# Optimization experiments

Measured on AMD Instinct MI355X. Metric: run time of the kernel, lower is better.

The kernel has to match this reference:

```python
import jax, jax.numpy as jnp
import numpy as np

HEAD_DIM = 128
NUM_HEADS = 16
NUM_KV_HEADS = 16
ROPE_MAX_POS = 4096
ROPE_BASE = 10000.0


def _rope_tables(seq_len):
    # cos/sin cached tables: [S, D/2]
    inv_freq = 1.0 / (ROPE_BASE ** (jnp.arange(0, HEAD_DIM, 2, dtype=jnp.float32) / HEAD_DIM))
    t = jnp.arange(seq_len, dtype=jnp.float32)
    freqs = jnp.outer(t, inv_freq)
    return jnp.cos(freqs), jnp.sin(freqs)


def _apply_rope(x, cos, sin):
    # x: [B, S, H, D]; cos/sin: [S, D/2] -> broadcast over heads as [S, 1, D/2]
    orig_dtype = x.dtype
    c = cos[:, None, :]
    s = sin[:, None, :]
    xf = x.astype(jnp.float32)
    x_real, x_im = jnp.split(xf, 2, axis=-1)  # half-split (not interleaved) RoPE
    x_real_e = x_real * c - x_im * s
    x_im_e = x_im * c + x_real * s
    return jnp.concatenate((x_real_e, x_im_e), axis=-1).astype(orig_dtype)


def setup_inputs() -> dict:
    key = jax.random.key(0)
    k1, k2, k3 = jax.random.split(key, 3)
    B, S, H = 1, 4096, 2048
    hidden_states = jax.random.normal(k1, (B, S, H), dtype=jnp.float32)
    # trunc-normal-ish init, std ~ 1/sqrt(fan_in)
    w_qkv = jax.random.normal(k2, ((NUM_HEADS + 2 * NUM_KV_HEADS) * HEAD_DIM, H), dtype=jnp.float32) / jnp.sqrt(jnp.float32(H))
    w_o = jax.random.normal(k3, (H, NUM_HEADS * HEAD_DIM), dtype=jnp.float32) / jnp.sqrt(jnp.float32(NUM_HEADS * HEAD_DIM))
    return {"hidden_states": hidden_states, "w_qkv": w_qkv, "w_o": w_o}


def reference(hidden_states, w_qkv, w_o):
    B, S, _ = hidden_states.shape
    qkv = jnp.einsum('bsh,oh->bso', hidden_states, w_qkv)
    qkv = qkv.reshape(B, S, NUM_HEADS + 2 * NUM_KV_HEADS, HEAD_DIM)
    q = qkv[:, :, :NUM_HEADS]
    k = qkv[:, :, NUM_HEADS:NUM_HEADS + NUM_KV_HEADS]
    v = qkv[:, :, NUM_HEADS + NUM_KV_HEADS:]

    cos, sin = _rope_tables(S)
    q = _apply_rope(q, cos, sin)
    k = _apply_rope(k, cos, sin)

    scale = 1.0 / jnp.sqrt(jnp.float32(HEAD_DIM)).astype(q.dtype)
    # scores: [B, H, Sq, Sk]
    scores = jnp.einsum('bqhd,bkhd->bhqk', q, k) * scale
    causal = jnp.tril(jnp.ones((S, S), dtype=bool))
    scores = jnp.where(causal[None, None], scores, jnp.finfo(scores.dtype).min)
    probs = jax.nn.softmax(scores, axis=-1)
    attn = jnp.einsum('bhqk,bkhd->bqhd', probs, v)
    attn = attn.reshape(B, S, NUM_HEADS * HEAD_DIM)
    return jnp.einsum('bso,ho->bsh', attn, w_o)
```

## Files before the change

### kernel.cpp

```cpp
#include <hip/hip_runtime.h>

typedef __bf16 bf16;
typedef __bf16 bf16x8 __attribute__((ext_vector_type(8)));
typedef __bf16 bf16x4 __attribute__((ext_vector_type(4)));
typedef float f32x4 __attribute__((ext_vector_type(4)));

#define SEQ 4096
#define QKV_LD 6144
#define HNUM 16

__device__ __forceinline__ void async16(const bf16* g, bf16* l) {
    __builtin_amdgcn_global_load_lds((const __attribute__((address_space(1))) void*)g,
                                     (__attribute__((address_space(3))) void*)l, 16, 0, 0);
}

__global__ __launch_bounds__(256) void prep(const float* __restrict__ X, bf16* __restrict__ Xb,
                                            const float* __restrict__ Wq, bf16* __restrict__ Wqb,
                                            const float* __restrict__ Wo, bf16* __restrict__ Wob,
                                            float* __restrict__ T) {
    const int b = blockIdx.x, t = threadIdx.x;
    if (b < 12288) {
        const float* src;
        bf16* dst;
        int off;
        if (b < 4096)       { src = X;  dst = Xb;  off = b; }
        else if (b < 10240) { src = Wq; dst = Wqb; off = b - 4096; }
        else                { src = Wo; dst = Wob; off = b - 10240; }
        int i = (off * 256 + t) * 8;
        f32x4 a = *(const f32x4*)(src + i);
        f32x4 c = *(const f32x4*)(src + i + 4);
        bf16x8 w;
#pragma unroll
        for (int j = 0; j < 4; j++) { w[j] = (bf16)a[j]; w[4 + j] = (bf16)c[j]; }
        *(bf16x8*)(dst + i) = w;
    } else {
        int i = (b - 12288) * 256 + t;
        int s = i >> 6, d = i & 63;
        float inv_freq = powf(10000.0f, -(float)d * (1.0f / 64.0f));
        float ang = (float)s * inv_freq;
        T[2 * i]     = cosf(ang);
        T[2 * i + 1] = sinf(ang);
    }
}

__device__ __forceinline__ bf16x8 ldfrag(const bf16* slot, int row, int qd) {
    int lin  = row * 64 + qd * 16;
    int phys = lin ^ (((lin >> 9) & 1) << 5);
    return *(const bf16x8*)((const char*)slot + phys);
}

#define STAGE2(SG, SGR0, STT, SKK, SBUF, SMAT)                                  \
    {                                                                           \
        int tcl = (STT) < NT ? (STT) : NT - 1;                                  \
        const bf16* gsrc = (SG) + (size_t)(SGR0)*K + tcl * 64 + (SKK)*32;       \
        bf16* sl = &LDS[SBUF][SMAT][SKK][0];                                    \
        async16(gsrc + g0, (bf16*)((char*)sl + lb0));                           \
        async16(gsrc + g1, (bf16*)((char*)sl + lb1));                           \
    }

#define PHASE(QM, KKI, LOADB, SG, SGR0, STT, SKK, SBUF, SMAT, DOVM)             \
    {                                                                           \
        if (LOADB) {                                                            \
            _Pragma("unroll") for (int j = 0; j < 4; j++)                       \
                bB[j] = ldfrag(&LDS[bi][1][KKI][0],                             \
                               (wc >> 1) * 128 + (wc & 1) * 32 +                \
                                   (j & 1) * 16 + (j >> 1) * 64 + ln, qd);      \
        }                                                                       \
        bf16x8 aA[4];                                                           \
        _Pragma("unroll") for (int i = 0; i < 4; i++)                           \
            aA[i] = ldfrag(&LDS[bi][0][KKI][0],                                 \
                           wr * 128 + (QM)*64 + i * 16 + ln, qd);               \
        STAGE2(SG, SGR0, STT, SKK, SBUF, SMAT);                                 \
        __builtin_amdgcn_sched_barrier(0);                                      \
        if (DOVM) {                                                             \
            asm volatile("s_waitcnt vmcnt(4)" ::: "memory");                    \
            __builtin_amdgcn_sched_barrier(0);                                  \
        }                                                                       \
        __builtin_amdgcn_s_barrier();                                           \
        __builtin_amdgcn_sched_barrier(0);                                      \
        __builtin_amdgcn_s_setprio(1);                                          \
        _Pragma("unroll") for (int i = 0; i < 4; i++)                           \
            _Pragma("unroll") for (int j = 0; j < 4; j++)                       \
                acc[(QM)*4 + i][j] = __builtin_amdgcn_mfma_f32_16x16x32_bf16(   \
                    aA[i], bB[j], acc[(QM)*4 + i][j], 0, 0, 0);                 \
        __builtin_amdgcn_s_setprio(0);                                          \
        __builtin_amdgcn_sched_barrier(0);                                      \
        __builtin_amdgcn_s_barrier();                                           \
        __builtin_amdgcn_sched_barrier(0);                                      \
    }

template <int ROPE>
__global__ __launch_bounds__(512, 2) void gemm256_nt(const bf16* __restrict__ A,
                                                     const bf16* __restrict__ B,
                                                     bf16* __restrict__ C,
                                                     int M, int N, int K,
                                                     const float* __restrict__ T) {
    __shared__ __align__(16) bf16 LDS[2][2][2][256 * 32];
    const int tid  = threadIdx.x;
    const int wave = tid >> 6, lane = tid & 63;
    const int qd = lane >> 4, ln = lane & 15;
    const int wr = wave >> 2, wc = wave & 3;
    const int bm = blockIdx.x * 256, bn = blockIdx.y * 256;
    const int NT = K >> 6;

    const int seg0 = wave * 2, seg1 = seg0 + 1;
    const int Pr0 = seg0 * 1024 + lane * 16;
    const int Pr1 = seg1 * 1024 + lane * 16;
    const int Lr0 = Pr0 ^ (((Pr0 >> 9) & 1) << 5);
    const int Lr1 = Pr1 ^ (((Pr1 >> 9) & 1) << 5);
    const size_t g0 = (size_t)(Lr0 >> 6) * K + ((Lr0 & 63) >> 1);
    const size_t g1 = (size_t)(Lr1 >> 6) * K + ((Lr1 & 63) >> 1);
    const int lb0 = seg0 * 1024, lb1 = seg1 * 1024;

    f32x4 acc[8][4] = {};

    STAGE2(A, bm, 0, 0, 0, 0);
    STAGE2(B, bn, 0, 0, 0, 1);
    STAGE2(A, bm, 0, 1, 0, 0);
    STAGE2(B, bn, 0, 1, 0, 1);
    STAGE2(A, bm, 1, 0, 1, 0);
    STAGE2(B, bn, 1, 0, 1, 1);
    __builtin_amdgcn_sched_barrier(0);
    asm volatile("s_waitcnt vmcnt(4)" ::: "memory");
    __builtin_amdgcn_sched_barrier(0);
    __builtin_amdgcn_s_barrier();
    __builtin_amdgcn_sched_barrier(0);

    for (int t = 0; t < NT; ++t) {
        const int bi = t & 1;
        bf16x8 bB[4];
        PHASE(0, 0, 1, A, bm, t + 1, 1, bi ^ 1, 0, 0)
        PHASE(1, 0, 0, B, bn, t + 1, 1, bi ^ 1, 1, 0)
        PHASE(0, 1, 1, A, bm, t + 2, 0, bi,     0, 0)
        PHASE(1, 1, 0, B, bn, t + 2, 0, bi,     1, 1)
    }
    asm volatile("s_waitcnt vmcnt(0)" ::: "memory");

    const int colb = bn + (wc >> 1) * 128 + (wc & 1) * 32 + ln;
    if (ROPE && bn < 4096) {
        const float2* T2 = (const float2*)T;
        const int d0 = (wc & 1) * 32 + ln;
#pragma unroll
        for (int mi = 0; mi < 8; mi++)
#pragma unroll
            for (int r = 0; r < 4; r++) {
                int row = bm + wr * 128 + mi * 16 + qd * 4 + r;
                float2 cs0 = T2[(size_t)row * 64 + d0];
                float2 cs1 = T2[(size_t)row * 64 + d0 + 16];
                float a0 = acc[mi][0][r], b0 = acc[mi][2][r];
                float a1 = acc[mi][1][r], b1 = acc[mi][3][r];
                size_t o = (size_t)row * N + colb;
                C[o]      = (bf16)(a0 * cs0.x - b0 * cs0.y);
                C[o + 64] = (bf16)(b0 * cs0.x + a0 * cs0.y);
                C[o + 16] = (bf16)(a1 * cs1.x - b1 * cs1.y);
                C[o + 80] = (bf16)(b1 * cs1.x + a1 * cs1.y);
            }
    } else if (ROPE) {
        bf16* Vb = C + 4096;
#pragma unroll
        for (int mi = 0; mi < 8; mi++) {
            const int row = bm + wr * 128 + mi * 16 + qd * 4;
            const int rhi = row >> 11;
            const int rlo = row & 2047;
#pragma unroll
            for (int j = 0; j < 4; j++) {
                const int dh = colb - 4096 + (j & 1) * 16 + (j >> 1) * 64;
                bf16x4 w;
#pragma unroll
                for (int r = 0; r < 4; r++) w[r] = (bf16)acc[mi][j][r];
                *(bf16x4*)(Vb + (size_t)(2 * dh + rhi) * N + rlo) = w;
            }
        }
    } else {
#pragma unroll
        for (int mi = 0; mi < 8; mi++)
#pragma unroll
            for (int r = 0; r < 4; r++) {
                size_t o = (size_t)(bm + wr * 128 + mi * 16 + qd * 4 + r) * N + colb;
                C[o]      = (bf16)acc[mi][0][r];
                C[o + 16] = (bf16)acc[mi][1][r];
                C[o + 64] = (bf16)acc[mi][2][r];
                C[o + 80] = (bf16)acc[mi][3][r];
            }
    }
}

__device__ __forceinline__ bf16x8 ldfragB(const bf16* slot, int row, int qd) {
    int lin  = row * 64 + qd * 16;
    int phys = lin ^ (((lin >> 9) & 1) << 5);
    return *(const bf16x8*)((const char*)slot + phys);
}

#define STG(TT, KKI, BUF)                                                      \
    {                                                                          \
        int tcl = (TT) < NT ? (TT) : NT - 1;                                   \
        const bf16* As = A + (size_t)bm * K + tcl * 64 + (KKI)*32;             \
        const bf16* Bs = B + (size_t)bn * K + tcl * 64 + (KKI)*32;             \
        async16(As + gA,  (bf16*)((char*)&LA[BUF][KKI][0] + lbA));             \
        async16(Bs + gB0, (bf16*)((char*)&LB[BUF][KKI][0] + lbB0));            \
        async16(Bs + gB1, (bf16*)((char*)&LB[BUF][KKI][0] + lbB1));            \
    }

#define PH(KKI, TT, SKK, SBUF, DOVM)                                           \
    {                                                                          \
        bf16x8 aA[4], bB[4];                                                   \
        _Pragma("unroll") for (int i = 0; i < 4; i++)                          \
            aA[i] = ldfragB(&LA[bi][KKI][0], wr * 64 + i * 16 + ln, qd);       \
        _Pragma("unroll") for (int j = 0; j < 4; j++)                          \
            bB[j] = ldfragB(&LB[bi][KKI][0], wc * 64 + j * 16 + ln, qd);       \
        STG(TT, SKK, SBUF);                                                    \
        __builtin_amdgcn_sched_barrier(0);                                     \
        if (DOVM) {                                                            \
            asm volatile("s_waitcnt vmcnt(3)" ::: "memory");                   \
            __builtin_amdgcn_sched_barrier(0);                                 \
        }                                                                      \
        __builtin_amdgcn_s_barrier();                                          \
        __builtin_amdgcn_sched_barrier(0);                                     \
        __builtin_amdgcn_s_setprio(1);                                         \
        _Pragma("unroll") for (int i = 0; i < 4; i++)                          \
            _Pragma("unroll") for (int j = 0; j < 4; j++)                      \
                acc[i][j] = __builtin_amdgcn_mfma_f32_16x16x32_bf16(           \
                    aA[i], bB[j], acc[i][j], 0, 0, 0);                         \
        __builtin_amdgcn_s_setprio(0);                                         \
        __builtin_amdgcn_sched_barrier(0);                                     \
        __builtin_amdgcn_s_barrier();                                          \
        __builtin_amdgcn_sched_barrier(0);                                     \
    }

template <int C_F32>
__global__ __launch_bounds__(512, 2) void gemm128x256(const bf16* __restrict__ A,
                                                      const bf16* __restrict__ B,
                                                      void* __restrict__ Cp,
                                                      int M, int N, int K) {
    __shared__ __align__(16) bf16 LA[2][2][128 * 32];
    __shared__ __align__(16) bf16 LB[2][2][256 * 32];
    const int tid  = threadIdx.x;
    const int wave = tid >> 6, lane = tid & 63;
    const int qd = lane >> 4, ln = lane & 15;
    const int wr = wave >> 2, wc = wave & 3;
    const int bm = blockIdx.x * 128, bn = blockIdx.y * 256;
    const int NT = K >> 6;

    const int PrA  = wave * 1024 + lane * 16;
    const int PrB0 = (2 * wave) * 1024 + lane * 16;
    const int PrB1 = PrB0 + 1024;
    const int LrA  = PrA  ^ (((PrA  >> 9) & 1) << 5);
    const int LrB0 = PrB0 ^ (((PrB0 >> 9) & 1) << 5);
    const int LrB1 = PrB1 ^ (((PrB1 >> 9) & 1) << 5);
    const size_t gA  = (size_t)(LrA  >> 6) * K + ((LrA  & 63) >> 1);
    const size_t gB0 = (size_t)(LrB0 >> 6) * K + ((LrB0 & 63) >> 1);
    const size_t gB1 = (size_t)(LrB1 >> 6) * K + ((LrB1 & 63) >> 1);
    const int lbA = wave * 1024, lbB0 = 2 * wave * 1024, lbB1 = lbB0 + 1024;

    f32x4 acc[4][4] = {};

    STG(0, 0, 0);
    STG(0, 1, 0);
    STG(1, 0, 1);
    __builtin_amdgcn_sched_barrier(0);
    asm volatile("s_waitcnt vmcnt(3)" ::: "memory");
    __builtin_amdgcn_sched_barrier(0);
    __builtin_amdgcn_s_barrier();
    __builtin_amdgcn_sched_barrier(0);

    for (int t = 0; t < NT; ++t) {
        const int bi = t & 1;
        PH(0, t + 1, 1, bi ^ 1, 0)
        PH(1, t + 2, 0, bi,     1)
    }
    asm volatile("s_waitcnt vmcnt(0)" ::: "memory");

    const size_t cb = (size_t)(bm + wr * 64 + qd * 4) * N + (bn + wc * 64 + ln);
#pragma unroll
    for (int mi = 0; mi < 4; mi++)
#pragma unroll
        for (int j = 0; j < 4; j++)
#pragma unroll
            for (int r = 0; r < 4; r++) {
                size_t idx = cb + (size_t)(mi * 16 + r) * N + j * 16;
                if (C_F32) ((float*)Cp)[idx] = acc[mi][j][r];
                else       ((bf16*)Cp)[idx]  = (bf16)acc[mi][j][r];
            }
}

template <int A_F32, int B_F32, int C_F32>
__global__ __launch_bounds__(256) void gemm_nt(const void* __restrict__ Ap,
                                               const void* __restrict__ Bp,
                                               void* __restrict__ Cp,
                                               int M, int N, int K) {
    __shared__ __align__(16) bf16 sA[128 * 32];
    __shared__ __align__(16) bf16 sB[128 * 32];
    const int tid  = threadIdx.x;
    const int wave = tid >> 6, lane = tid & 63;
    const int qd = lane >> 4, ln = lane & 15;
    const int bm = blockIdx.x * 128, bn = blockIdx.y * 128;
    const int wm = (wave >> 1) * 64, wn = (wave & 1) * 64;

    const int srow = wave * 16 + (lane >> 2);
    const int scol = (lane & 3) * 8;
    const size_t rowoff = (size_t)srow * K + scol;
    const size_t rowskip = (size_t)64 * K;

    const bf16* Ab = (const bf16*)Ap + (size_t)bm * K + rowoff;
    const bf16* Bb = (const bf16*)Bp + (size_t)bn * K + rowoff;
    const float* Af = (const float*)Ap + (size_t)bm * K + rowoff;
    const float* Bf = (const float*)Bp + (size_t)bn * K + rowoff;
    bf16* sAd0 = &sA[(wave * 16) * 32];
    bf16* sAd1 = &sA[(64 + wave * 16) * 32];
    bf16* sBd0 = &sB[(wave * 16) * 32];
    bf16* sBd1 = &sB[(64 + wave * 16) * 32];
    bf16* sAw0 = &sA[srow * 32 + scol];
    bf16* sAw1 = &sA[(64 + srow) * 32 + scol];
    bf16* sBw0 = &sB[srow * 32 + scol];
    bf16* sBw1 = &sB[(64 + srow) * 32 + scol];

    f32x4 acc[4][4] = {};
    for (int k0 = 0; k0 < K; k0 += 32) {
        if (A_F32) {
            f32x4 u0 = *(const f32x4*)(Af + k0);
            f32x4 u1 = *(const f32x4*)(Af + k0 + 4);
            f32x4 u2 = *(const f32x4*)(Af + rowskip + k0);
            f32x4 u3 = *(const f32x4*)(Af + rowskip + k0 + 4);
            bf16x8 w0, w1;
#pragma unroll
            for (int i = 0; i < 4; i++) { w0[i] = (bf16)u0[i]; w0[4 + i] = (bf16)u1[i];
                                          w1[i] = (bf16)u2[i]; w1[4 + i] = (bf16)u3[i]; }
            *(bf16x8*)sAw0 = w0;
            *(bf16x8*)sAw1 = w1;
        } else {
            async16(Ab + k0, sAd0);
            async16(Ab + rowskip + k0, sAd1);
        }
        if (B_F32) {
            f32x4 u0 = *(const f32x4*)(Bf + k0);
            f32x4 u1 = *(const f32x4*)(Bf + k0 + 4);
            f32x4 u2 = *(const f32x4*)(Bf + rowskip + k0);
            f32x4 u3 = *(const f32x4*)(Bf + rowskip + k0 + 4);
            bf16x8 w0, w1;
#pragma unroll
            for (int i = 0; i < 4; i++) { w0[i] = (bf16)u0[i]; w0[4 + i] = (bf16)u1[i];
                                          w1[i] = (bf16)u2[i]; w1[4 + i] = (bf16)u3[i]; }
            *(bf16x8*)sBw0 = w0;
            *(bf16x8*)sBw1 = w1;
        } else {
            async16(Bb + k0, sBd0);
            async16(Bb + rowskip + k0, sBd1);
        }
        __syncthreads();
        bf16x8 af[4], bfr[4];
#pragma unroll
        for (int i = 0; i < 4; i++)
            af[i] = *(const bf16x8*)&sA[(wm + i * 16 + ln) * 32 + qd * 8];
#pragma unroll
        for (int j = 0; j < 4; j++)
            bfr[j] = *(const bf16x8*)&sB[(wn + j * 16 + ln) * 32 + qd * 8];
#pragma unroll
        for (int i = 0; i < 4; i++)
#pragma unroll
            for (int j = 0; j < 4; j++)
                acc[i][j] = __builtin_amdgcn_mfma_f32_16x16x32_bf16(af[i], bfr[j], acc[i][j], 0, 0, 0);
        __syncthreads();
    }
    const size_t cbase = (size_t)(bm + wm + qd * 4) * N + (bn + wn + ln);
#pragma unroll
    for (int i = 0; i < 4; i++)
#pragma unroll
        for (int j = 0; j < 4; j++)
#pragma unroll
            for (int r = 0; r < 4; r++) {
                size_t idx = cbase + (size_t)(i * 16 + r) * N + j * 16;
                if (C_F32) ((float*)Cp)[idx] = acc[i][j][r];
                else       ((bf16*)Cp)[idx] = (bf16)acc[i][j][r];
            }
}

__global__ __launch_bounds__(256) void rope_k_inline(bf16* __restrict__ QKV) {
    const int s  = blockIdx.x;
    const int t  = threadIdx.x;
    const int hh = (blockIdx.y << 2) + (t >> 6);
    const int d  = t & 63;
    bf16* p = QKV + (size_t)s * QKV_LD + hh * 128 + d;
    float x0 = (float)p[0];
    float x1 = (float)p[64];
    float inv_freq = powf(10000.0f, -(float)d * (1.0f / 64.0f));
    float ang = (float)s * inv_freq;
    float c = cosf(ang), sn = sinf(ang);
    p[0]  = (bf16)(x0 * c - x1 * sn);
    p[64] = (bf16)(x1 * c + x0 * sn);
}

template <int USE_VT>
__global__ __launch_bounds__(256, 2) void flash_attn(const bf16* __restrict__ QKV,
                                                     bf16* __restrict__ O) {
    __shared__ __align__(16) bf16 sK[64 * 128];
    __shared__ __align__(16) bf16 sV[128 * 64];
    __shared__ __align__(16) bf16 sP[4][32 * 64];
    const int tid  = threadIdx.x;
    const int wave = tid >> 6, lane = tid & 63;
    const int qd = lane >> 4, ln = lane & 15;
    const int h  = blockIdx.x;
    const int y  = blockIdx.y;
    const int qtile = (y < 16) ? (31 - y) : (y - 16);
    const int qw0 = qtile * 128 + wave * 32;
    const int nkv = 2 * qtile + 2;
    const float scale = 0.08838834764831843f;

    bf16x8 Qf[2][4];
#pragma unroll
    for (int qt = 0; qt < 2; qt++) {
        const bf16* Qg = QKV + (size_t)(qw0 + qt * 16 + ln) * QKV_LD + h * 128;
#pragma unroll
        for (int ks = 0; ks < 4; ks++) {
            bf16x8 q8 = *(const bf16x8*)(Qg + ks * 32 + qd * 8);
#pragma unroll
            for (int e = 0; e < 8; e++) q8[e] = (bf16)((float)q8[e] * scale);
            Qf[qt][ks] = q8;
        }
    }

    f32x4 Oacc[2][8] = {};
    float l_i[2] = {0.0f, 0.0f};

    const int krow = tid >> 4;
    const int kblk = tid & 15;
    const int vrow = tid >> 3;
    const int vblk = tid & 7;
    const int vd   = tid & 127;
    const int vh   = tid >> 7;
    const bf16* Kg  = QKV + 2048 + h * 128;
    const bf16* Vg  = QKV + 4096 + h * 128;
    const bf16* Vtb = QKV + 4096;

    bf16x8 Kpre[4], Vpre[4];
#pragma unroll
    for (int rr = 0; rr < 4; rr++)
        Kpre[rr] = *(const bf16x8*)(Kg + (size_t)(rr * 16 + krow) * QKV_LD + kblk * 8);
    if (USE_VT) {
#pragma unroll
        for (int u = 0; u < 4; u++) {
            int dh = h * 128 + u * 32 + vrow;
            Vpre[u] = *(const bf16x8*)(Vtb + (size_t)(2 * dh) * QKV_LD + vblk * 8);
        }
    } else {
#pragma unroll
        for (int u = 0; u < 4; u++)
#pragma unroll
            for (int j = 0; j < 8; j++)
                Vpre[u][j] = Vg[(size_t)(vh * 32 + u * 8 + j) * QKV_LD + vd];
    }

    for (int kt = 0; kt < nkv; kt++) {
        const int kbase = kt * 64;
#pragma unroll
        for (int rr = 0; rr < 4; rr++) {
            int kv = rr * 16 + krow;
            *(bf16x8*)&sK[kv * 128 + ((kblk ^ (kv & 7)) * 8)] = Kpre[rr];
        }
        if (USE_VT) {
#pragma unroll
            for (int u = 0; u < 4; u++) {
                int d = u * 32 + vrow;
                *(bf16x8*)&sV[d * 64 + ((vblk ^ (d & 7)) * 8)] = Vpre[u];
            }
        } else {
#pragma unroll
            for (int u = 0; u < 4; u++)
                *(bf16x8*)&sV[vd * 64 + (((vh * 4 + u) ^ (vd & 7)) * 8)] = Vpre[u];
        }
        __syncthreads();
        if (kt + 1 < nkv) {
            const int nb = kbase + 64;
#pragma unroll
            for (int rr = 0; rr < 4; rr++)
                Kpre[rr] = *(const bf16x8*)(Kg + (size_t)(nb + rr * 16 + krow) * QKV_LD + kblk * 8);
            if (USE_VT) {
#pragma unroll
                for (int u = 0; u < 4; u++) {
                    int dh = h * 128 + u * 32 + vrow;
                    Vpre[u] = *(const bf16x8*)(Vtb + (size_t)(2 * dh + (nb >> 11)) * QKV_LD +
                                               (nb & 2047) + vblk * 8);
                }
            } else {
#pragma unroll
                for (int u = 0; u < 4; u++)
#pragma unroll
                    for (int j = 0; j < 8; j++)
                        Vpre[u][j] = Vg[(size_t)(nb + vh * 32 + u * 8 + j) * QKV_LD + vd];
            }
        }
        if (kbase <= qw0 + 31) {
            f32x4 Sacc[2][4] = {};
            __builtin_amdgcn_s_setprio(1);
#pragma unroll
            for (int ks = 0; ks < 4; ks++)
#pragma unroll
                for (int j = 0; j < 4; j++) {
                    bf16x8 af = *(const bf16x8*)&sK[(j * 16 + ln) * 128 + (((ks * 4 + qd) ^ (ln & 7)) * 8)];
                    Sacc[0][j] = __builtin_amdgcn_mfma_f32_16x16x32_bf16(af, Qf[0][ks], Sacc[0][j], 0, 0, 0);
                    Sacc[1][j] = __builtin_amdgcn_mfma_f32_16x16x32_bf16(af, Qf[1][ks], Sacc[1][j], 0, 0, 0);
                }
            __builtin_amdgcn_s_setprio(0);
#pragma unroll
            for (int qt = 0; qt < 2; qt++) {
                const int qs = qw0 + qt * 16;
                if (kbase + 63 > qs) {
#pragma unroll
                    for (int j = 0; j < 4; j++)
#pragma unroll
                        for (int r = 0; r < 4; r++)
                            if (kbase + j * 16 + qd * 4 + r > qs + ln) Sacc[qt][j][r] = -1e30f;
                }
                float psum = 0.0f;
#pragma unroll
                for (int j = 0; j < 4; j++) {
                    bf16x4 p4;
#pragma unroll
                    for (int r = 0; r < 4; r++) {
                        float p = __expf(Sacc[qt][j][r]);
                        psum += p;
                        p4[r] = (bf16)p;
                    }
                    int blk = (j * 2 + (qd >> 1)) ^ (ln & 7);
                    *(bf16x4*)&sP[wave][(qt * 16 + ln) * 64 + blk * 8 + (qd & 1) * 4] = p4;
                }
                psum += __shfl_xor(psum, 16);
                psum += __shfl_xor(psum, 32);
                l_i[qt] += psum;
            }
            __builtin_amdgcn_s_setprio(1);
#pragma unroll
            for (int ks = 0; ks < 2; ks++) {
                bf16x8 pf0 = *(const bf16x8*)&sP[wave][(0 * 16 + ln) * 64 + (((ks * 4 + qd) ^ (ln & 7)) * 8)];
                bf16x8 pf1 = *(const bf16x8*)&sP[wave][(1 * 16 + ln) * 64 + (((ks * 4 + qd) ^ (ln & 7)) * 8)];
#pragma unroll
                for (int dt = 0; dt < 8; dt++) {
                    bf16x8 vf = *(const bf16x8*)&sV[(dt * 16 + ln) * 64 + (((ks * 4 + qd) ^ (ln & 7)) * 8)];
                    Oacc[0][dt] = __builtin_amdgcn_mfma_f32_16x16x32_bf16(pf0, vf, Oacc[0][dt], 0, 0, 0);
                    Oacc[1][dt] = __builtin_amdgcn_mfma_f32_16x16x32_bf16(pf1, vf, Oacc[1][dt], 0, 0, 0);
                }
            }
            __builtin_amdgcn_s_setprio(0);
        }
        __syncthreads();
    }
#pragma unroll
    for (int qt = 0; qt < 2; qt++) {
        float linv[4];
#pragma unroll
        for (int r = 0; r < 4; r++)
            linv[r] = 1.0f / __shfl(l_i[qt], (lane & 48) | (qd * 4 + r));
        bf16* Ob = O + (size_t)(qw0 + qt * 16 + qd * 4) * 2048 + h * 128 + ln;
#pragma unroll
        for (int dt = 0; dt < 8; dt++)
#pragma unroll
            for (int r = 0; r < 4; r++)
                Ob[(size_t)r * 2048 + dt * 16] = (bf16)(Oacc[qt][dt][r] * linv[r]);
    }
}

extern "C" void kernel_launch(void* const* d_in, const int* in_sizes, int n_in,
                              void* d_out, int out_size, void* d_ws, size_t ws_size,
                              hipStream_t stream) {
    const float* X    = (const float*)d_in[0];
    const float* Wqkv = (const float*)d_in[1];
    const float* Wo   = (const float*)d_in[2];
    float* out = (float*)d_out;
    bf16* QKV = (bf16*)d_ws;
    bf16* ATT = QKV + (size_t)4096 * 6144;

    const size_t nX = (size_t)4096 * 2048, nWq = (size_t)6144 * 2048, nWo = (size_t)2048 * 2048;
    const size_t need = (nX * 3 + nWq * 2 + nWo) * 2 + nX * 2;

    if (ws_size >= need) {
        bf16* Xb  = ATT + nX;
        bf16* Wqb = Xb + nX;
        bf16* Wob = Wqb + nWq;
        float* Tab = (float*)ATT;
        prep<<<13312, 256, 0, stream>>>(X, Xb, Wqkv, Wqb, Wo, Wob, Tab);
        gemm256_nt<1><<<dim3(16, 24), 512, 0, stream>>>(Xb, Wqb, QKV, 4096, 6144, 2048, Tab);
        flash_attn<1><<<dim3(HNUM, 32), 256, 0, stream>>>(QKV, ATT);
        gemm128x256<1><<<dim3(32, 8), 512, 0, stream>>>(ATT, Wob, out, 4096, 2048, 2048);
    } else {
        gemm_nt<1, 1, 0><<<dim3(32, 48), 256, 0, stream>>>(X, Wqkv, QKV, 4096, 6144, 2048);
        rope_k_inline<<<dim3(4096, 8), 256, 0, stream>>>(QKV);
        flash_attn<0><<<dim3(HNUM, 32), 256, 0, stream>>>(QKV, ATT);
        gemm_nt<0, 1, 1><<<dim3(32, 16), 256, 0, stream>>>(ATT, Wo, out, 4096, 2048, 2048);
    }
}
```

Before: 401.0 us.

## Halve GEMM K-tile to 32 with a two-phase pipeline and raise occupancy target

Shrinks each K-step of the bf16 GEMM mainloop from 64 to 32. LDS drops to a single K-slice per buffer, half the previous size. The loop body becomes two phases, each issuing one async global-to-LDS stage and 16 MFMAs. The launch bound asks for 4 blocks of 512 threads per CU to raise occupancy. That bound caps registers per wave well below the 128-register accumulator plus fragments, so the compiler may spill heavily, and smaller K-steps raise the barrier rate per unit of work.

```diff
diff --git a/kernel.cpp b/kernel.cpp
--- a/kernel.cpp
+++ b/kernel.cpp
@@ -49,59 +49,28 @@
     return *(const bf16x8*)((const char*)slot + phys);
 }
 
-#define STAGE2(SG, SGR0, STT, SKK, SBUF, SMAT)                                  \
+#define STAGE1(SG, SGR0, STT, SBUF, SMAT)                                       \
     {                                                                           \
         int tcl = (STT) < NT ? (STT) : NT - 1;                                  \
-        const bf16* gsrc = (SG) + (size_t)(SGR0)*K + tcl * 64 + (SKK)*32;       \
-        bf16* sl = &LDS[SBUF][SMAT][SKK][0];                                    \
+        const bf16* gsrc = (SG) + (size_t)(SGR0)*K + tcl * 32;                  \
+        bf16* sl = &LDS[SBUF][SMAT][0];                                         \
         async16(gsrc + g0, (bf16*)((char*)sl + lb0));                           \
         async16(gsrc + g1, (bf16*)((char*)sl + lb1));                           \
     }
 
-#define PHASE(QM, KKI, LOADB, SG, SGR0, STT, SKK, SBUF, SMAT, DOVM)             \
-    {                                                                           \
-        if (LOADB) {                                                            \
-            _Pragma("unroll") for (int j = 0; j < 4; j++)                       \
-                bB[j] = ldfrag(&LDS[bi][1][KKI][0],                             \
-                               (wc >> 1) * 128 + (wc & 1) * 32 +                \
-                                   (j & 1) * 16 + (j >> 1) * 64 + ln, qd);      \
-        }                                                                       \
-        bf16x8 aA[4];                                                           \
-        _Pragma("unroll") for (int i = 0; i < 4; i++)                           \
-            aA[i] = ldfrag(&LDS[bi][0][KKI][0],                                 \
-                           wr * 128 + (QM)*64 + i * 16 + ln, qd);               \
-        STAGE2(SG, SGR0, STT, SKK, SBUF, SMAT);                                 \
-        __builtin_amdgcn_sched_barrier(0);                                      \
-        if (DOVM) {                                                             \
-            asm volatile("s_waitcnt vmcnt(4)" ::: "memory");                    \
-            __builtin_amdgcn_sched_barrier(0);                                  \
-        }                                                                       \
-        __builtin_amdgcn_s_barrier();                                           \
-        __builtin_amdgcn_sched_barrier(0);                                      \
-        __builtin_amdgcn_s_setprio(1);                                          \
-        _Pragma("unroll") for (int i = 0; i < 4; i++)                           \
-            _Pragma("unroll") for (int j = 0; j < 4; j++)                       \
-                acc[(QM)*4 + i][j] = __builtin_amdgcn_mfma_f32_16x16x32_bf16(   \
-                    aA[i], bB[j], acc[(QM)*4 + i][j], 0, 0, 0);                 \
-        __builtin_amdgcn_s_setprio(0);                                          \
-        __builtin_amdgcn_sched_barrier(0);                                      \
-        __builtin_amdgcn_s_barrier();                                           \
-        __builtin_amdgcn_sched_barrier(0);                                      \
-    }
-
 template <int ROPE>
-__global__ __launch_bounds__(512, 2) void gemm256_nt(const bf16* __restrict__ A,
+__global__ __launch_bounds__(512, 4) void gemm256_nt(const bf16* __restrict__ A,
                                                      const bf16* __restrict__ B,
                                                      bf16* __restrict__ C,
                                                      int M, int N, int K,
                                                      const float* __restrict__ T) {
-    __shared__ __align__(16) bf16 LDS[2][2][2][256 * 32];
+    __shared__ __align__(16) bf16 LDS[2][2][256 * 32];
     const int tid  = threadIdx.x;
     const int wave = tid >> 6, lane = tid & 63;
     const int qd = lane >> 4, ln = lane & 15;
     const int wr = wave >> 2, wc = wave & 3;
     const int bm = blockIdx.x * 256, bn = blockIdx.y * 256;
-    const int NT = K >> 6;
+    const int NT = K >> 5;
 
     const int seg0 = wave * 2, seg1 = seg0 + 1;
     const int Pr0 = seg0 * 1024 + lane * 16;
@@ -114,12 +83,10 @@
 
     f32x4 acc[8][4] = {};
 
-    STAGE2(A, bm, 0, 0, 0, 0);
-    STAGE2(B, bn, 0, 0, 0, 1);
-    STAGE2(A, bm, 0, 1, 0, 0);
-    STAGE2(B, bn, 0, 1, 0, 1);
-    STAGE2(A, bm, 1, 0, 1, 0);
-    STAGE2(B, bn, 1, 0, 1, 1);
+    STAGE1(B, bn, 0, 0, 1);
+    STAGE1(A, bm, 0, 0, 0);
+    STAGE1(B, bn, 1, 1, 1);
+    STAGE1(A, bm, 1, 1, 0);
     __builtin_amdgcn_sched_barrier(0);
     asm volatile("s_waitcnt vmcnt(4)" ::: "memory");
     __builtin_amdgcn_sched_barrier(0);
@@ -128,11 +95,47 @@
 
     for (int t = 0; t < NT; ++t) {
         const int bi = t & 1;
-        bf16x8 bB[4];
-        PHASE(0, 0, 1, A, bm, t + 1, 1, bi ^ 1, 0, 0)
-        PHASE(1, 0, 0, B, bn, t + 1, 1, bi ^ 1, 1, 0)
-        PHASE(0, 1, 1, A, bm, t + 2, 0, bi,     0, 0)
-        PHASE(1, 1, 0, B, bn, t + 2, 0, bi,     1, 1)
+        bf16x8 bB[4], aA[4];
+#pragma unroll
+        for (int j = 0; j < 4; j++)
+            bB[j] = ldfrag(&LDS[bi][1][0],
+                           (wc >> 1) * 128 + (wc & 1) * 32 + (j & 1) * 16 + (j >> 1) * 64 + ln, qd);
+#pragma unroll
+        for (int i = 0; i < 4; i++)
+            aA[i] = ldfrag(&LDS[bi][0][0], wr * 128 + i * 16 + ln, qd);
+        __builtin_amdgcn_sched_barrier(0);
+        __builtin_amdgcn_s_barrier();
+        __builtin_amdgcn_sched_barrier(0);
+        STAGE1(B, bn, t + 2, bi, 1);
+        __builtin_amdgcn_sched_barrier(0);
+        __builtin_amdgcn_s_setprio(1);
+#pragma unroll
+        for (int i = 0; i < 4; i++)
+#pragma unroll
+            for (int j = 0; j < 4; j++)
+                acc[i][j] = __builtin_amdgcn_mfma_f32_16x16x32_bf16(aA[i], bB[j], acc[i][j], 0, 0, 0);
+        __builtin_amdgcn_s_setprio(0);
+        __builtin_amdgcn_sched_barrier(0);
+#pragma unroll
+        for (int i = 0; i < 4; i++)
+            aA[i] = ldfrag(&LDS[bi][0][0], wr * 128 + 64 + i * 16 + ln, qd);
+        __builtin_amdgcn_sched_barrier(0);
+        __builtin_amdgcn_s_barrier();
+        __builtin_amdgcn_sched_barrier(0);
+        STAGE1(A, bm, t + 2, bi, 0);
+        __builtin_amdgcn_sched_barrier(0);
+        __builtin_amdgcn_s_setprio(1);
+#pragma unroll
+        for (int i = 0; i < 4; i++)
+#pragma unroll
+            for (int j = 0; j < 4; j++)
+                acc[4 + i][j] = __builtin_amdgcn_mfma_f32_16x16x32_bf16(aA[i], bB[j], acc[4 + i][j], 0, 0, 0);
+        __builtin_amdgcn_s_setprio(0);
+        __builtin_amdgcn_sched_barrier(0);
+        asm volatile("s_waitcnt vmcnt(4)" ::: "memory");
+        __builtin_amdgcn_sched_barrier(0);
+        __builtin_amdgcn_s_barrier();
+        __builtin_amdgcn_sched_barrier(0);
     }
     asm volatile("s_waitcnt vmcnt(0)" ::: "memory");
 
```

New measurement: 1.132 ms. 2.82x slower.
